# Performance work log

Measured on AMD Instinct MI355X. Metric: run time of the kernel, lower is better.

Reference implementation:

```python
import jax, jax.numpy as jnp
import numpy as np
import math

B, T, E, H, HS = 8, 2048, 384, 6, 64

def setup_inputs() -> dict:
    key = jax.random.key(0)
    ks = jax.random.split(key, 5)
    scale = 1.0 / math.sqrt(E)
    return {
        "x": jax.random.normal(ks[0], (B, T, E), dtype=jnp.float32),
        "Wq": jax.random.normal(ks[1], (H, E, HS), dtype=jnp.float32) * scale,
        "Wk": jax.random.normal(ks[2], (H, E, HS), dtype=jnp.float32) * scale,
        "Wv": jax.random.normal(ks[3], (H, E, HS), dtype=jnp.float32) * scale,
        "Wo": jax.random.normal(ks[4], (H, HS, E), dtype=jnp.float32) * (1.0 / math.sqrt(HS)),
    }

def reference(x, Wq, Wk, Wv, Wo):
    # x: [B,T,E]; per-head projections batched over heads.
    q = jnp.einsum('bte,hed->bhtd', x, Wq)  # [B,H,T,HS]
    k = jnp.einsum('bte,hed->bhtd', x, Wk)
    v = jnp.einsum('bte,hed->bhtd', x, Wv)
    scores = jnp.einsum('bhid,bhjd->bhij', q, k)  # [B,H,T,T]
    # Faithful to source: MULTIPLICATIVE tril mask (masked logits become 0, not -inf),
    # then scale by 1/sqrt(head_size), then softmax.
    t = x.shape[1]
    tril = jnp.tril(jnp.ones((t, t), dtype=scores.dtype))
    scores = scores * tril / math.sqrt(HS)
    attn = jax.nn.softmax(scores, axis=-1)
    ctx = jnp.einsum('bhij,bhjd->bhid', attn, v)  # [B,H,T,HS]
    # Per-head output projection to embed dim, summed over heads (source accumulates).
    out = jnp.einsum('bhtd,hde->bte', ctx, Wo)  # [B,T,E]
    return out
```

## Files before the change

### kernel.cpp

```cpp
#include <hip/hip_runtime.h>
#include <math.h>

#define BBATCH 8
#define TSEQ   2048
#define EDIM   384
#define NHEAD  6
#define DHEAD  64
#define NBH    48
#define QTILE  128
#define NQT    16
#define NW1    442368
#define NW2    147456
#define XSZ    6291456
#define KVSZ   6291456

typedef __attribute__((ext_vector_type(8)))  short bf16x8;
typedef __attribute__((ext_vector_type(16))) float f32x16;
typedef __attribute__((ext_vector_type(2)))  int   i32x2;
typedef unsigned short u16;
typedef unsigned int   u32;

#define MFMA(a, b, c) __builtin_amdgcn_mfma_f32_32x32x16_bf16(a, b, c, 0, 0, 0)

__device__ __forceinline__ u16 f2bf(float f) {
  u32 u = __float_as_uint(f);
  return (u16)((u + 0x7fffu + ((u >> 16) & 1u)) >> 16);
}
__device__ __forceinline__ float bf2f(u16 h) {
  return __uint_as_float(((u32)h) << 16);
}
__device__ __forceinline__ bf16x8 mk8(u32 w0, u32 w1, u32 w2, u32 w3) {
  union { u32 u[4]; bf16x8 v; } t;
  t.u[0] = w0; t.u[1] = w1; t.u[2] = w2; t.u[3] = w3;
  return t.v;
}

__global__ __launch_bounds__(256) void prep_w_k(
    const float* __restrict__ Wq, const float* __restrict__ Wk,
    const float* __restrict__ Wv, const float* __restrict__ Wo,
    u16* __restrict__ wtH, u16* __restrict__ wtL,
    u16* __restrict__ woH, u16* __restrict__ woL) {
  int idx = blockIdx.x * 256 + threadIdx.x;
  if (idx < NW1) {
    int d = idx & 63;
    int q = idx >> 6;
    int e = q % EDIM;
    int ph = q / EDIM;
    const float* W = (ph < 6) ? Wq : (ph < 12) ? Wk : Wv;
    int h = ph % 6;
    float v = W[((size_t)h * EDIM + e) * DHEAD + d];
    u16 hi = f2bf(v);
    size_t o = ((size_t)ph * DHEAD + d) * EDIM + e;
    wtH[o] = hi;
    wtL[o] = f2bf(v - bf2f(hi));
  } else {
    int o = idx - NW1;
    int eo = o % EDIM;
    int hd = o / EDIM;
    float v = Wo[(size_t)hd * EDIM + eo];
    u16 hi = f2bf(v);
    size_t oo = (size_t)eo * EDIM + hd;
    woH[oo] = hi;
    woL[oo] = f2bf(v - bf2f(hi));
  }
}

__global__ __launch_bounds__(256) void splitx_k(
    const float* __restrict__ x, u16* __restrict__ xh, u16* __restrict__ xl) {
  int i = (blockIdx.x * 256 + threadIdx.x) * 8;
  float4 a = *(const float4*)(x + i);
  float4 b = *(const float4*)(x + i + 4);
  u16 h0 = f2bf(a.x), h1 = f2bf(a.y), h2 = f2bf(a.z), h3 = f2bf(a.w);
  u16 h4 = f2bf(b.x), h5 = f2bf(b.y), h6 = f2bf(b.z), h7 = f2bf(b.w);
  uint4 H, L;
  H.x = (u32)h0 | ((u32)h1 << 16); H.y = (u32)h2 | ((u32)h3 << 16);
  H.z = (u32)h4 | ((u32)h5 << 16); H.w = (u32)h6 | ((u32)h7 << 16);
  L.x = (u32)f2bf(a.x - bf2f(h0)) | ((u32)f2bf(a.y - bf2f(h1)) << 16);
  L.y = (u32)f2bf(a.z - bf2f(h2)) | ((u32)f2bf(a.w - bf2f(h3)) << 16);
  L.z = (u32)f2bf(b.x - bf2f(h4)) | ((u32)f2bf(b.y - bf2f(h5)) << 16);
  L.w = (u32)f2bf(b.z - bf2f(h6)) | ((u32)f2bf(b.w - bf2f(h7)) << 16);
  *(uint4*)(xh + i) = H;
  *(uint4*)(xl + i) = L;
}

__global__ __launch_bounds__(256, 2) void proj_k(
    const u16* __restrict__ xh, const u16* __restrict__ xl,
    const u16* __restrict__ wtH, const u16* __restrict__ wtL,
    u16* __restrict__ qh, u16* __restrict__ ql,
    u16* __restrict__ kh, u16* __restrict__ kl,
    u16* __restrict__ vTh, u16* __restrict__ vTl) {
  __shared__ __align__(16) unsigned char sm[32768];
  const int tid = threadIdx.x;
  const int w = tid >> 6, l = tid & 63, lh = l >> 5, l31 = l & 31;
  const int gid = ((blockIdx.x & 7) * 288) + ((int)blockIdx.x >> 3);
  const int bx = gid / 18, ph = gid % 18;
  const int p = ph / 6, h = ph % 6;
  const int bt0 = bx * 128;
  const u16* __restrict__ wBh = wtH + (size_t)ph * DHEAD * EDIM;
  const u16* __restrict__ wBl = wtL + (size_t)ph * DHEAD * EDIM;

  f32x16 acc0, acc1;
#pragma unroll
  for (int i = 0; i < 16; ++i) { acc0[i] = 0.f; acc1[i] = 0.f; }

  for (int k0 = 0; k0 < EDIM; k0 += 64) {
    __syncthreads();
#pragma unroll
    for (int i = 0; i < 4; ++i) {
      int c = tid + i * 256;
      int r = c >> 3, s = c & 7;
      int off = (r * 128 + s * 16) ^ ((r & 7) << 4);
      size_t g = (size_t)(bt0 + r) * EDIM + k0 + s * 8;
      *(uint4*)(sm + off) = *(const uint4*)(xh + g);
      *(uint4*)(sm + 16384 + off) = *(const uint4*)(xl + g);
    }
    __syncthreads();
    const int arow = 32 * w + l31;
#pragma unroll
    for (int ks = 0; ks < 4; ++ks) {
      int aoff = (arow * 128 + ks * 32 + 16 * lh) ^ ((arow & 7) << 4);
      bf16x8 aH = *(const bf16x8*)(sm + aoff);
      bf16x8 aL = *(const bf16x8*)(sm + 16384 + aoff);
      int eoff = k0 + ks * 16 + 8 * lh;
      size_t b0 = (size_t)l31 * EDIM + eoff;
      size_t b1 = (size_t)(32 + l31) * EDIM + eoff;
      bf16x8 bH0 = *(const bf16x8*)(wBh + b0);
      bf16x8 bL0 = *(const bf16x8*)(wBl + b0);
      bf16x8 bH1 = *(const bf16x8*)(wBh + b1);
      bf16x8 bL1 = *(const bf16x8*)(wBl + b1);
      acc0 = MFMA(aH, bH0, acc0); acc0 = MFMA(aH, bL0, acc0); acc0 = MFMA(aL, bH0, acc0);
      acc1 = MFMA(aH, bH1, acc1); acc1 = MFMA(aH, bL1, acc1); acc1 = MFMA(aL, bH1, acc1);
    }
  }

  const int b = bt0 >> 11, t0b = bt0 & (TSEQ - 1);
  const int bh = b * NHEAD + h;
  const float scale = (p == 0) ? 0.125f : 1.0f;

  if (p < 2) {
    u16* oH = (p == 0) ? qh : kh;
    u16* oL = (p == 0) ? ql : kl;
#pragma unroll
    for (int reg = 0; reg < 16; ++reg) {
      int row = (reg & 3) + 8 * (reg >> 2) + 4 * lh + 32 * w;
      size_t base = ((size_t)bh * TSEQ + t0b + row) * DHEAD;
      float v0 = acc0[reg] * scale, v1 = acc1[reg] * scale;
      u16 h0 = f2bf(v0), h1 = f2bf(v1);
      oH[base + l31] = h0;       oL[base + l31] = f2bf(v0 - bf2f(h0));
      oH[base + 32 + l31] = h1;  oL[base + 32 + l31] = f2bf(v1 - bf2f(h1));
    }
  } else {
    u16* T = (u16*)sm;
#pragma unroll
    for (int half = 0; half < 2; ++half) {
      __syncthreads();
#pragma unroll
      for (int reg = 0; reg < 16; ++reg) {
        int t = (reg & 3) + 8 * (reg >> 2) + 4 * lh + 32 * w;
        float v0 = acc0[reg], v1 = acc1[reg];
        u16 e0, e1;
        if (half == 0) { e0 = f2bf(v0); e1 = f2bf(v1); }
        else {
          u16 a0 = f2bf(v0), a1 = f2bf(v1);
          e0 = f2bf(v0 - bf2f(a0)); e1 = f2bf(v1 - bf2f(a1));
        }
        T[l31 * 132 + t] = e0;
        T[(32 + l31) * 132 + t] = e1;
      }
      __syncthreads();
      u16* dst = half ? vTl : vTh;
#pragma unroll
      for (int i = 0; i < 8; ++i) {
        int c = tid + i * 256;
        int d = c >> 5, s = c & 31;
        uint2 val = *(const uint2*)(T + d * 132 + s * 4);
        *(uint2*)(dst + ((size_t)bh * DHEAD + d) * TSEQ + t0b + s * 4) = val;
      }
    }
  }
}

__global__ __launch_bounds__(256) void vsuffix_k(
    const u16* __restrict__ vTh, const u16* __restrict__ vTl,
    float* __restrict__ vsuf) {
  __shared__ float psum[NQT][DHEAD];
  const int bh = blockIdx.x, tid = threadIdx.x;
  const int d = tid >> 2, seg = tid & 3;
  const size_t rb = ((size_t)bh * DHEAD + d) * TSEQ;
#pragma unroll
  for (int tl = 0; tl < 4; ++tl) {
    float s = 0.f;
    int t0 = seg * 512 + tl * 128;
#pragma unroll
    for (int c = 0; c < 16; ++c) {
      uint4 H = *(const uint4*)(vTh + rb + t0 + c * 8);
      uint4 L = *(const uint4*)(vTl + rb + t0 + c * 8);
      const u32* hw = (const u32*)&H;
      const u32* lw = (const u32*)&L;
#pragma unroll
      for (int k = 0; k < 4; ++k) {
        s += bf2f((u16)(hw[k] & 0xffffu)) + bf2f((u16)(hw[k] >> 16));
        s += bf2f((u16)(lw[k] & 0xffffu)) + bf2f((u16)(lw[k] >> 16));
      }
    }
    psum[seg * 4 + tl][d] = s;
  }
  __syncthreads();
  if (tid < 64) {
    float s = 0.f;
    for (int q = NQT - 1; q >= 0; --q) {
      vsuf[((size_t)bh * NQT + q) * DHEAD + tid] = s;
      s += psum[q][tid];
    }
  }
}

__global__ __launch_bounds__(256, 3) void attn_k(
    const u16* __restrict__ qh, const u16* __restrict__ ql,
    const u16* __restrict__ kh, const u16* __restrict__ kl,
    const u16* __restrict__ vTh, const u16* __restrict__ vTl,
    const float* __restrict__ vsuf,
    u16* __restrict__ cxh, u16* __restrict__ cxl) {
  __shared__ __align__(16) unsigned char sm[32768];
  const int oKl = 8192, oVh = 16384, oVl = 24576;
  const int tid = threadIdx.x;
  const int w = tid >> 6, l = tid & 63, lh = l >> 5, l31 = l & 31;
  const int gid = ((blockIdx.x & 7) * 96) + ((int)blockIdx.x >> 3);
  const int bh = gid >> 4;
  const int qt = (NQT - 1) - (gid & 15);
  const int b = bh / NHEAD, h = bh % NHEAD;
  const int t0 = qt * QTILE;
  const size_t kvb = (size_t)bh * TSEQ * DHEAD;

#pragma unroll
  for (int i = 0; i < 4; ++i) {
    int c = tid + i * 256;
    int r = c >> 3, s = c & 7;
    int off = (r * 128 + s * 16) ^ ((r & 7) << 4);
    size_t g = kvb + (size_t)(t0 + r) * DHEAD + s * 8;
    *(uint4*)(sm + off) = *(const uint4*)(qh + g);
    *(uint4*)(sm + 16384 + off) = *(const uint4*)(ql + g);
  }
  __syncthreads();
  bf16x8 qfH[4], qfL[4];
  {
    const int qrow = 32 * w + l31;
#pragma unroll
    for (int ks = 0; ks < 4; ++ks) {
      int off = (qrow * 128 + ks * 32 + 16 * lh) ^ ((qrow & 7) << 4);
      qfH[ks] = *(const bf16x8*)(sm + off);
      qfL[ks] = *(const bf16x8*)(sm + 16384 + off);
    }
  }
  uint4 kpH[2], kpL[2], vpH[2], vpL[2];
#pragma unroll
  for (int i = 0; i < 2; ++i) {
    int c = tid + i * 256;
    int r = c >> 3, s = c & 7;
    kpH[i] = *(const uint4*)(kh + kvb + (size_t)r * DHEAD + s * 8);
    kpL[i] = *(const uint4*)(kl + kvb + (size_t)r * DHEAD + s * 8);
    vpH[i] = *(const uint4*)(vTh + kvb + (size_t)r * TSEQ + s * 8);
    vpL[i] = *(const uint4*)(vTl + kvb + (size_t)r * TSEQ + s * 8);
  }
  __syncthreads();

  f32x16 accO0, accO1;
#pragma unroll
  for (int i = 0; i < 16; ++i) { accO0[i] = 0.f; accO1[i] = 0.f; }
  float lrun = 0.f;
  const int qg = t0 + 32 * w + l31;
  const int S = 2 * (qt + 1);

  for (int jt = 0; jt < S; ++jt) {
#pragma unroll
    for (int i = 0; i < 2; ++i) {
      int c = tid + i * 256;
      int r = c >> 3, s = c & 7;
      int off = (r * 128 + s * 16) ^ ((r & 7) << 4);
      *(uint4*)(sm + off) = kpH[i];
      *(uint4*)(sm + oKl + off) = kpL[i];
      *(uint4*)(sm + oVh + off) = vpH[i];
      *(uint4*)(sm + oVl + off) = vpL[i];
    }
    __syncthreads();
    if (jt + 1 < S) {
      int j0 = (jt + 1) * 64;
#pragma unroll
      for (int i = 0; i < 2; ++i) {
        int c = tid + i * 256;
        int r = c >> 3, s = c & 7;
        kpH[i] = *(const uint4*)(kh + kvb + (size_t)(j0 + r) * DHEAD + s * 8);
        kpL[i] = *(const uint4*)(kl + kvb + (size_t)(j0 + r) * DHEAD + s * 8);
        vpH[i] = *(const uint4*)(vTh + kvb + (size_t)r * TSEQ + j0 + s * 8);
        vpL[i] = *(const uint4*)(vTl + kvb + (size_t)r * TSEQ + j0 + s * 8);
      }
    }
#pragma unroll
    for (int jh = 0; jh < 2; ++jh) {
      f32x16 accS;
#pragma unroll
      for (int i = 0; i < 16; ++i) accS[i] = 0.f;
      const int krow = jh * 32 + l31;
      const int ksw = (l31 & 7) << 4;
#pragma unroll
      for (int ks = 0; ks < 4; ++ks) {
        int koff = (krow * 128 + ks * 32 + 16 * lh) ^ ksw;
        bf16x8 aH = *(const bf16x8*)(sm + koff);
        bf16x8 aL = *(const bf16x8*)(sm + oKl + koff);
        accS = MFMA(aH, qfH[ks], accS);
        accS = MFMA(aH, qfL[ks], accS);
        accS = MFMA(aL, qfH[ks], accS);
      }
      const int jb = jt * 64 + jh * 32 + 4 * lh;
      float ps = 0.f;
#pragma unroll
      for (int ml = 0; ml < 2; ++ml) {
        int rb = ml * 8;
        u32 hw[4], lw[4];
#pragma unroll
        for (int pr = 0; pr < 4; ++pr) {
          int r0 = rb + 2 * pr;
          int jg0 = jb + (r0 & 3) + 8 * (r0 >> 2);
          float s0 = (jg0 > qg) ? 0.f : accS[r0];
          float s1 = ((jg0 + 1) > qg) ? 0.f : accS[r0 + 1];
          float p0 = __expf(s0), p1 = __expf(s1);
          ps += p0 + p1;
          u16 a0 = f2bf(p0), a1 = f2bf(p1);
          hw[pr] = (u32)a0 | ((u32)a1 << 16);
          lw[pr] = (u32)f2bf(p0 - bf2f(a0)) | ((u32)f2bf(p1 - bf2f(a1)) << 16);
        }
        i32x2 s1 = __builtin_amdgcn_permlane32_swap((int)hw[0], (int)hw[2], false, false);
        i32x2 s2 = __builtin_amdgcn_permlane32_swap((int)hw[1], (int)hw[3], false, false);
        bf16x8 pH = mk8((u32)s1.x, (u32)s2.x, (u32)s1.y, (u32)s2.y);
        i32x2 t1 = __builtin_amdgcn_permlane32_swap((int)lw[0], (int)lw[2], false, false);
        i32x2 t2 = __builtin_amdgcn_permlane32_swap((int)lw[1], (int)lw[3], false, false);
        bf16x8 pL = mk8((u32)t1.x, (u32)t2.x, (u32)t1.y, (u32)t2.y);
        int m = jh * 2 + ml;
        int vo0 = (l31 * 128 + m * 32 + 16 * lh) ^ ksw;
        int vo1 = ((32 + l31) * 128 + m * 32 + 16 * lh) ^ ksw;
        bf16x8 vH0 = *(const bf16x8*)(sm + oVh + vo0);
        bf16x8 vL0 = *(const bf16x8*)(sm + oVl + vo0);
        bf16x8 vH1 = *(const bf16x8*)(sm + oVh + vo1);
        bf16x8 vL1 = *(const bf16x8*)(sm + oVl + vo1);
        accO0 = MFMA(pH, vH0, accO0); accO0 = MFMA(pH, vL0, accO0); accO0 = MFMA(pL, vH0, accO0);
        accO1 = MFMA(pH, vH1, accO1); accO1 = MFMA(pH, vL1, accO1); accO1 = MFMA(pL, vH1, accO1);
      }
      lrun += ps;
    }
    __syncthreads();
  }

  lrun += __shfl_xor(lrun, 32);
  lrun += (float)(TSEQ - S * 64);
  {
    const float* vs = vsuf + ((size_t)bh * NQT + qt) * DHEAD;
    float s0 = vs[l31], s1 = vs[32 + l31];
#pragma unroll
    for (int reg = 0; reg < 16; ++reg) { accO0[reg] += s0; accO1[reg] += s1; }
  }
#pragma unroll
  for (int reg = 0; reg < 16; ++reg) {
    int qrow = (reg & 3) + 8 * (reg >> 2) + 4 * lh;
    float lq = __shfl(lrun, qrow);
    float inv = 1.f / lq;
    int t = t0 + 32 * w + qrow;
    size_t o = ((size_t)b * TSEQ + t) * EDIM + h * DHEAD;
    float v0 = accO0[reg] * inv, v1 = accO1[reg] * inv;
    u16 h0 = f2bf(v0), h1 = f2bf(v1);
    cxh[o + l31] = h0;       cxl[o + l31] = f2bf(v0 - bf2f(h0));
    cxh[o + 32 + l31] = h1;  cxl[o + 32 + l31] = f2bf(v1 - bf2f(h1));
  }
}

__global__ __launch_bounds__(256, 2) void outproj_k(
    const u16* __restrict__ cxh, const u16* __restrict__ cxl,
    const u16* __restrict__ woH, const u16* __restrict__ woL,
    float* __restrict__ out) {
  __shared__ __align__(16) unsigned char sm[32768];
  const int tid = threadIdx.x;
  const int w = tid >> 6, l = tid & 63, lh = l >> 5, l31 = l & 31;
  const int gid = ((blockIdx.x & 7) * 96) + ((int)blockIdx.x >> 3);
  const int bx = gid / 6, ey = gid % 6;
  const int bt0 = bx * 128, e0 = ey * 64;

  f32x16 acc0, acc1;
#pragma unroll
  for (int i = 0; i < 16; ++i) { acc0[i] = 0.f; acc1[i] = 0.f; }

  for (int k0 = 0; k0 < EDIM; k0 += 64) {
    __syncthreads();
#pragma unroll
    for (int i = 0; i < 4; ++i) {
      int c = tid + i * 256;
      int r = c >> 3, s = c & 7;
      int off = (r * 128 + s * 16) ^ ((r & 7) << 4);
      size_t g = (size_t)(bt0 + r) * EDIM + k0 + s * 8;
      *(uint4*)(sm + off) = *(const uint4*)(cxh + g);
      *(uint4*)(sm + 16384 + off) = *(const uint4*)(cxl + g);
    }
    __syncthreads();
    const int arow = 32 * w + l31;
#pragma unroll
    for (int ks = 0; ks < 4; ++ks) {
      int aoff = (arow * 128 + ks * 32 + 16 * lh) ^ ((arow & 7) << 4);
      bf16x8 aH = *(const bf16x8*)(sm + aoff);
      bf16x8 aL = *(const bf16x8*)(sm + 16384 + aoff);
      int hdoff = k0 + ks * 16 + 8 * lh;
      size_t b0 = (size_t)(e0 + l31) * EDIM + hdoff;
      size_t b1 = (size_t)(e0 + 32 + l31) * EDIM + hdoff;
      bf16x8 bH0 = *(const bf16x8*)(woH + b0);
      bf16x8 bL0 = *(const bf16x8*)(woL + b0);
      bf16x8 bH1 = *(const bf16x8*)(woH + b1);
      bf16x8 bL1 = *(const bf16x8*)(woL + b1);
      acc0 = MFMA(aH, bH0, acc0); acc0 = MFMA(aH, bL0, acc0); acc0 = MFMA(aL, bH0, acc0);
      acc1 = MFMA(aH, bH1, acc1); acc1 = MFMA(aH, bL1, acc1); acc1 = MFMA(aL, bH1, acc1);
    }
  }
#pragma unroll
  for (int reg = 0; reg < 16; ++reg) {
    int row = (reg & 3) + 8 * (reg >> 2) + 4 * lh + 32 * w;
    size_t o = (size_t)(bt0 + row) * EDIM + e0;
    out[o + l31] = acc0[reg];
    out[o + 32 + l31] = acc1[reg];
  }
}

extern "C" void kernel_launch(void* const* d_in, const int* in_sizes, int n_in,
                              void* d_out, int out_size, void* d_ws, size_t ws_size,
                              hipStream_t stream) {
  (void)in_sizes; (void)n_in; (void)out_size; (void)ws_size;
  const float* x  = (const float*)d_in[0];
  const float* Wq = (const float*)d_in[1];
  const float* Wk = (const float*)d_in[2];
  const float* Wv = (const float*)d_in[3];
  const float* Wo = (const float*)d_in[4];
  float* out = (float*)d_out;

  u16* qh  = (u16*)d_ws;
  u16* ql  = qh + KVSZ;
  u16* kh  = ql + KVSZ;
  u16* kl  = kh + KVSZ;
  u16* vTh = kl + KVSZ;
  u16* vTl = vTh + KVSZ;
  u16* xh  = vTl + KVSZ;
  u16* xl  = xh + XSZ;
  u16* wtH = xl + XSZ;
  u16* wtL = wtH + NW1;
  u16* woH = wtL + NW1;
  u16* woL = woH + NW2;
  float* vsuf = (float*)(woL + NW2);
  u16* cxh = xh;
  u16* cxl = xl;

  hipLaunchKernelGGL(prep_w_k, dim3((NW1 + NW2) / 256), dim3(256), 0, stream,
                     Wq, Wk, Wv, Wo, wtH, wtL, woH, woL);
  hipLaunchKernelGGL(splitx_k, dim3(XSZ / 2048), dim3(256), 0, stream, x, xh, xl);
  hipLaunchKernelGGL(proj_k, dim3(2304), dim3(256), 0, stream,
                     xh, xl, wtH, wtL, qh, ql, kh, kl, vTh, vTl);
  hipLaunchKernelGGL(vsuffix_k, dim3(NBH), dim3(256), 0, stream, vTh, vTl, vsuf);
  hipLaunchKernelGGL(attn_k, dim3(768), dim3(256), 0, stream,
                     qh, ql, kh, kl, vTh, vTl, vsuf, cxh, cxl);
  hipLaunchKernelGGL(outproj_k, dim3(768), dim3(256), 0, stream,
                     cxh, cxl, woH, woL, out);
}
```

Measured before the change: 529.8 us.

## Split causal attention KV range into balanced chunks with atomic partial combine

Attention work is split into 40 slots per batch-head, each covering at most eight 64-key tiles of one query tile, so long query tiles no longer dominate the tail. Partial outputs and row sums are accumulated with float atomics into zeroed buffers, and a new combine kernel adds the masked-tail V sum, normalizes, and writes the bf16 hi/lo context. The separate vsuffix kernel is removed; per-tile V sums are now computed inside the projection kernel. MFMA sections get raised wave priority and occupancy goes to 4 blocks per CU. The cost is extra atomic traffic, a memset, and another launch.

```diff
diff --git a/kernel.cpp b/kernel.cpp
--- a/kernel.cpp
+++ b/kernel.cpp
@@ -13,6 +13,7 @@
 #define NW2    147456
 #define XSZ    6291456
 #define KVSZ   6291456
+#define NSLOT  40
 
 typedef __attribute__((ext_vector_type(8)))  short bf16x8;
 typedef __attribute__((ext_vector_type(16))) float f32x16;
@@ -34,6 +35,13 @@
   t.u[0] = w0; t.u[1] = w1; t.u[2] = w2; t.u[3] = w3;
   return t.v;
 }
+
+__device__ const unsigned char SLOT_QT[NSLOT] = {
+  3,4,5,6,7,7,8,8,9,9,10,10,11,11,11,12,12,12,13,13,13,14,14,14,15,15,15,15,
+  2,6,10,14, 1,5,9,13, 0,4,8,12};
+__device__ const unsigned char SLOT_C[NSLOT] = {
+  0,0,0,0,0,1,0,1,0,1,0,1,0,1,2,0,1,2,0,1,2,0,1,2,0,1,2,3,
+  0,1,2,3, 0,1,2,3, 0,1,2,3};
 
 __global__ __launch_bounds__(256) void prep_w_k(
     const float* __restrict__ Wq, const float* __restrict__ Wk,
@@ -88,7 +96,8 @@
     const u16* __restrict__ wtH, const u16* __restrict__ wtL,
     u16* __restrict__ qh, u16* __restrict__ ql,
     u16* __restrict__ kh, u16* __restrict__ kl,
-    u16* __restrict__ vTh, u16* __restrict__ vTl) {
+    u16* __restrict__ vTh, u16* __restrict__ vTl,
+    float* __restrict__ psum) {
   __shared__ __align__(16) unsigned char sm[32768];
   const int tid = threadIdx.x;
   const int w = tid >> 6, l = tid & 63, lh = l >> 5, l31 = l & 31;
@@ -177,58 +186,37 @@
         *(uint2*)(dst + ((size_t)bh * DHEAD + d) * TSEQ + t0b + s * 4) = val;
       }
     }
-  }
-}
-
-__global__ __launch_bounds__(256) void vsuffix_k(
-    const u16* __restrict__ vTh, const u16* __restrict__ vTl,
-    float* __restrict__ vsuf) {
-  __shared__ float psum[NQT][DHEAD];
-  const int bh = blockIdx.x, tid = threadIdx.x;
-  const int d = tid >> 2, seg = tid & 3;
-  const size_t rb = ((size_t)bh * DHEAD + d) * TSEQ;
-#pragma unroll
-  for (int tl = 0; tl < 4; ++tl) {
-    float s = 0.f;
-    int t0 = seg * 512 + tl * 128;
-#pragma unroll
-    for (int c = 0; c < 16; ++c) {
-      uint4 H = *(const uint4*)(vTh + rb + t0 + c * 8);
-      uint4 L = *(const uint4*)(vTl + rb + t0 + c * 8);
-      const u32* hw = (const u32*)&H;
-      const u32* lw = (const u32*)&L;
-#pragma unroll
-      for (int k = 0; k < 4; ++k) {
-        s += bf2f((u16)(hw[k] & 0xffffu)) + bf2f((u16)(hw[k] >> 16));
-        s += bf2f((u16)(lw[k] & 0xffffu)) + bf2f((u16)(lw[k] >> 16));
-      }
-    }
-    psum[seg * 4 + tl][d] = s;
-  }
-  __syncthreads();
-  if (tid < 64) {
-    float s = 0.f;
-    for (int q = NQT - 1; q >= 0; --q) {
-      vsuf[((size_t)bh * NQT + q) * DHEAD + tid] = s;
-      s += psum[q][tid];
-    }
-  }
-}
-
-__global__ __launch_bounds__(256, 3) void attn_k(
+    float s0 = 0.f, s1 = 0.f;
+#pragma unroll
+    for (int reg = 0; reg < 16; ++reg) { s0 += acc0[reg]; s1 += acc1[reg]; }
+    s0 += __shfl_xor(s0, 32);
+    s1 += __shfl_xor(s1, 32);
+    __syncthreads();
+    float* ps = (float*)sm;
+    if (lh == 0) { ps[w * 64 + l31] = s0; ps[w * 64 + 32 + l31] = s1; }
+    __syncthreads();
+    if (tid < 64) {
+      float t = ps[tid] + ps[64 + tid] + ps[128 + tid] + ps[192 + tid];
+      int tile = t0b >> 7;
+      psum[((size_t)bh * NQT + tile) * DHEAD + tid] = t;
+    }
+  }
+}
+
+__global__ __launch_bounds__(256, 4) void attn_k(
     const u16* __restrict__ qh, const u16* __restrict__ ql,
     const u16* __restrict__ kh, const u16* __restrict__ kl,
     const u16* __restrict__ vTh, const u16* __restrict__ vTl,
-    const float* __restrict__ vsuf,
-    u16* __restrict__ cxh, u16* __restrict__ cxl) {
+    float* __restrict__ pO, float* __restrict__ pl) {
   __shared__ __align__(16) unsigned char sm[32768];
   const int oKl = 8192, oVh = 16384, oVl = 24576;
   const int tid = threadIdx.x;
   const int w = tid >> 6, l = tid & 63, lh = l >> 5, l31 = l & 31;
-  const int gid = ((blockIdx.x & 7) * 96) + ((int)blockIdx.x >> 3);
-  const int bh = gid >> 4;
-  const int qt = (NQT - 1) - (gid & 15);
-  const int b = bh / NHEAD, h = bh % NHEAD;
+  const int gid = ((blockIdx.x & 7) * 240) + ((int)blockIdx.x >> 3);
+  const int bh = gid / NSLOT, slot = gid % NSLOT;
+  const int qt = SLOT_QT[slot], cch = SLOT_C[slot];
+  const int tbeg = cch * 8;
+  const int tend = min(cch * 8 + 8, 2 * qt + 2);
   const int t0 = qt * QTILE;
   const size_t kvb = (size_t)bh * TSEQ * DHEAD;
 
@@ -257,10 +245,11 @@
   for (int i = 0; i < 2; ++i) {
     int c = tid + i * 256;
     int r = c >> 3, s = c & 7;
-    kpH[i] = *(const uint4*)(kh + kvb + (size_t)r * DHEAD + s * 8);
-    kpL[i] = *(const uint4*)(kl + kvb + (size_t)r * DHEAD + s * 8);
-    vpH[i] = *(const uint4*)(vTh + kvb + (size_t)r * TSEQ + s * 8);
-    vpL[i] = *(const uint4*)(vTl + kvb + (size_t)r * TSEQ + s * 8);
+    int j0 = tbeg * 64;
+    kpH[i] = *(const uint4*)(kh + kvb + (size_t)(j0 + r) * DHEAD + s * 8);
+    kpL[i] = *(const uint4*)(kl + kvb + (size_t)(j0 + r) * DHEAD + s * 8);
+    vpH[i] = *(const uint4*)(vTh + kvb + (size_t)r * TSEQ + j0 + s * 8);
+    vpL[i] = *(const uint4*)(vTl + kvb + (size_t)r * TSEQ + j0 + s * 8);
   }
   __syncthreads();
 
@@ -269,9 +258,8 @@
   for (int i = 0; i < 16; ++i) { accO0[i] = 0.f; accO1[i] = 0.f; }
   float lrun = 0.f;
   const int qg = t0 + 32 * w + l31;
-  const int S = 2 * (qt + 1);
-
-  for (int jt = 0; jt < S; ++jt) {
+
+  for (int jt = tbeg; jt < tend; ++jt) {
 #pragma unroll
     for (int i = 0; i < 2; ++i) {
       int c = tid + i * 256;
@@ -283,7 +271,7 @@
       *(uint4*)(sm + oVl + off) = vpL[i];
     }
     __syncthreads();
-    if (jt + 1 < S) {
+    if (jt + 1 < tend) {
       int j0 = (jt + 1) * 64;
 #pragma unroll
       for (int i = 0; i < 2; ++i) {
@@ -302,6 +290,7 @@
       for (int i = 0; i < 16; ++i) accS[i] = 0.f;
       const int krow = jh * 32 + l31;
       const int ksw = (l31 & 7) << 4;
+      __builtin_amdgcn_s_setprio(1);
 #pragma unroll
       for (int ks = 0; ks < 4; ++ks) {
         int koff = (krow * 128 + ks * 32 + 16 * lh) ^ ksw;
@@ -311,6 +300,7 @@
         accS = MFMA(aH, qfL[ks], accS);
         accS = MFMA(aL, qfH[ks], accS);
       }
+      __builtin_amdgcn_s_setprio(0);
       const int jb = jt * 64 + jh * 32 + 4 * lh;
       float ps = 0.f;
 #pragma unroll
@@ -342,8 +332,10 @@
         bf16x8 vL0 = *(const bf16x8*)(sm + oVl + vo0);
         bf16x8 vH1 = *(const bf16x8*)(sm + oVh + vo1);
         bf16x8 vL1 = *(const bf16x8*)(sm + oVl + vo1);
+        __builtin_amdgcn_s_setprio(1);
         accO0 = MFMA(pH, vH0, accO0); accO0 = MFMA(pH, vL0, accO0); accO0 = MFMA(pL, vH0, accO0);
         accO1 = MFMA(pH, vH1, accO1); accO1 = MFMA(pH, vL1, accO1); accO1 = MFMA(pL, vH1, accO1);
+        __builtin_amdgcn_s_setprio(0);
       }
       lrun += ps;
     }
@@ -351,24 +343,42 @@
   }
 
   lrun += __shfl_xor(lrun, 32);
-  lrun += (float)(TSEQ - S * 64);
-  {
-    const float* vs = vsuf + ((size_t)bh * NQT + qt) * DHEAD;
-    float s0 = vs[l31], s1 = vs[32 + l31];
-#pragma unroll
-    for (int reg = 0; reg < 16; ++reg) { accO0[reg] += s0; accO1[reg] += s1; }
-  }
+  const size_t slotO = ((size_t)bh * NQT + qt);
+  if (lh == 0)
+    atomicAdd(&pl[slotO * 128 + 32 * w + l31], lrun);
+  float* po = pO + slotO * 8192;
 #pragma unroll
   for (int reg = 0; reg < 16; ++reg) {
-    int qrow = (reg & 3) + 8 * (reg >> 2) + 4 * lh;
-    float lq = __shfl(lrun, qrow);
-    float inv = 1.f / lq;
-    int t = t0 + 32 * w + qrow;
-    size_t o = ((size_t)b * TSEQ + t) * EDIM + h * DHEAD;
-    float v0 = accO0[reg] * inv, v1 = accO1[reg] * inv;
-    u16 h0 = f2bf(v0), h1 = f2bf(v1);
-    cxh[o + l31] = h0;       cxl[o + l31] = f2bf(v0 - bf2f(h0));
-    cxh[o + 32 + l31] = h1;  cxl[o + 32 + l31] = f2bf(v1 - bf2f(h1));
+    int r = (reg & 3) + 8 * (reg >> 2) + 4 * lh + 32 * w;
+    atomicAdd(&po[r * 64 + l31], accO0[reg]);
+    atomicAdd(&po[r * 64 + 32 + l31], accO1[reg]);
+  }
+}
+
+__global__ __launch_bounds__(256) void combine_k(
+    const float* __restrict__ pO, const float* __restrict__ pl,
+    const float* __restrict__ psum,
+    u16* __restrict__ cxh, u16* __restrict__ cxl) {
+  const int bid = blockIdx.x;
+  const int bh = bid >> 4, qt = bid & 15;
+  const int b = bh / NHEAD, h = bh % NHEAD;
+  const int tid = threadIdx.x;
+  const int d = tid & 63, rg = tid >> 6;
+  float tail = 0.f;
+  for (int tt = qt + 1; tt < NQT; ++tt)
+    tail += psum[((size_t)bh * NQT + tt) * DHEAD + d];
+  const float tcnt = (float)(TSEQ - (qt + 1) * 128);
+  const float* po = pO + (size_t)bid * 8192;
+  const float* plp = pl + (size_t)bid * 128;
+#pragma unroll 4
+  for (int k = 0; k < 32; ++k) {
+    int r = rg * 32 + k;
+    float inv = 1.0f / (plp[r] + tcnt);
+    float v = (po[r * 64 + d] + tail) * inv;
+    u16 hbits = f2bf(v);
+    size_t o = ((size_t)b * TSEQ + qt * 128 + r) * EDIM + h * DHEAD + d;
+    cxh[o] = hbits;
+    cxl[o] = f2bf(v - bf2f(hbits));
   }
 }
 
@@ -448,18 +458,22 @@
   u16* wtL = wtH + NW1;
   u16* woH = wtL + NW1;
   u16* woL = woH + NW2;
-  float* vsuf = (float*)(woL + NW2);
+  float* psum = (float*)(woL + NW2);
+  float* pO   = psum + (size_t)NBH * NQT * DHEAD;
+  float* pl   = pO + (size_t)NBH * NQT * 128 * 64;
   u16* cxh = xh;
   u16* cxl = xl;
 
+  hipMemsetAsync(pO, 0, ((size_t)NBH * NQT * 128 * 65) * sizeof(float), stream);
   hipLaunchKernelGGL(prep_w_k, dim3((NW1 + NW2) / 256), dim3(256), 0, stream,
                      Wq, Wk, Wv, Wo, wtH, wtL, woH, woL);
   hipLaunchKernelGGL(splitx_k, dim3(XSZ / 2048), dim3(256), 0, stream, x, xh, xl);
   hipLaunchKernelGGL(proj_k, dim3(2304), dim3(256), 0, stream,
-                     xh, xl, wtH, wtL, qh, ql, kh, kl, vTh, vTl);
-  hipLaunchKernelGGL(vsuffix_k, dim3(NBH), dim3(256), 0, stream, vTh, vTl, vsuf);
-  hipLaunchKernelGGL(attn_k, dim3(768), dim3(256), 0, stream,
-                     qh, ql, kh, kl, vTh, vTl, vsuf, cxh, cxl);
+                     xh, xl, wtH, wtL, qh, ql, kh, kl, vTh, vTl, psum);
+  hipLaunchKernelGGL(attn_k, dim3(1920), dim3(256), 0, stream,
+                     qh, ql, kh, kl, vTh, vTl, pO, pl);
+  hipLaunchKernelGGL(combine_k, dim3(NBH * NQT), dim3(256), 0, stream,
+                     pO, pl, psum, cxh, cxl);
   hipLaunchKernelGGL(outproj_k, dim3(768), dim3(256), 0, stream,
                      cxh, cxl, woH, woL, out);
 }
```

Result: slower. 551.2 us (+4.1%).
